# Optimization experiments

Measured on AMD Instinct MI355X. Metric: run time of the kernel, lower is better.

## Reference

```python
import jax, jax.numpy as jnp
import numpy as np

N_SRC = 20000
N_TGT = 20000
N_EDGE = 320000
D = 128            # in_dim == hid_dim
EDGE_IN = 2 * D + 1  # src feat + tgt feat + radial
COORD_MAX = 10.0


def _mlp2(x, w1, b1, w2, b2):
    # Linear -> SiLU -> Linear -> SiLU (edge MLP)
    h = jax.nn.silu(x @ w1 + b1)
    return jax.nn.silu(h @ w2 + b2)


def setup_inputs() -> dict:
    key = jax.random.key(0)
    ks = jax.random.split(key, 32)
    s = 0.05
    inp = {
        "src_node_feat": jax.random.normal(ks[0], (N_SRC, D), jnp.float32),
        "tgt_node_feat": jax.random.normal(ks[1], (N_TGT, D), jnp.float32),
        "src_node_coord": jax.random.normal(ks[2], (N_SRC, 3), jnp.float32),
        "tgt_node_coord": jax.random.normal(ks[3], (N_TGT, 3), jnp.float32),
        "edge_src": jax.random.randint(ks[4], (N_EDGE,), 0, N_SRC, jnp.int32),
        "edge_tgt": jax.random.randint(ks[5], (N_EDGE,), 0, N_TGT, jnp.int32),
        # edge MLP s2t
        "w1_s2t": jax.random.normal(ks[6], (EDGE_IN, D), jnp.float32) * s,
        "b1_s2t": jnp.zeros((D,), jnp.float32),
        "w2_s2t": jax.random.normal(ks[7], (D, D), jnp.float32) * s,
        "b2_s2t": jnp.zeros((D,), jnp.float32),
        # edge MLP t2s
        "w1_t2s": jax.random.normal(ks[8], (EDGE_IN, D), jnp.float32) * s,
        "b1_t2s": jnp.zeros((D,), jnp.float32),
        "w2_t2s": jax.random.normal(ks[9], (D, D), jnp.float32) * s,
        "b2_t2s": jnp.zeros((D,), jnp.float32),
        # gate MLPs (Linear(D,1) + Sigmoid)
        "wg_s2t": jax.random.normal(ks[10], (D, 1), jnp.float32) * s,
        "bg_s2t": jnp.zeros((1,), jnp.float32),
        "wg_t2s": jax.random.normal(ks[11], (D, 1), jnp.float32) * s,
        "bg_t2s": jnp.zeros((1,), jnp.float32),
        # coord MLP: Linear(D,D) + SiLU + Linear(D,1, bias=False, xavier gain 1e-3)
        "wc1": jax.random.normal(ks[12], (D, D), jnp.float32) * s,
        "bc1": jnp.zeros((D,), jnp.float32),
        "wc2": jax.random.normal(ks[13], (D, 1), jnp.float32) * 0.001,
        # node MLP tgt: Linear(2D,D) + SiLU + Linear(D,D)
        "wn1_t": jax.random.normal(ks[14], (2 * D, D), jnp.float32) * s,
        "bn1_t": jnp.zeros((D,), jnp.float32),
        "wn2_t": jax.random.normal(ks[15], (D, D), jnp.float32) * s,
        "bn2_t": jnp.zeros((D,), jnp.float32),
        # node MLP src
        "wn1_s": jax.random.normal(ks[16], (2 * D, D), jnp.float32) * s,
        "bn1_s": jnp.zeros((D,), jnp.float32),
        "wn2_s": jax.random.normal(ks[17], (D, D), jnp.float32) * s,
        "bn2_s": jnp.zeros((D,), jnp.float32),
    }
    return inp


def reference(src_node_feat, tgt_node_feat, src_node_coord, tgt_node_coord,
              edge_src, edge_tgt,
              w1_s2t, b1_s2t, w2_s2t, b2_s2t,
              w1_t2s, b1_t2s, w2_t2s, b2_t2s,
              wg_s2t, bg_s2t, wg_t2s, bg_t2s,
              wc1, bc1, wc2,
              wn1_t, bn1_t, wn2_t, bn2_t,
              wn1_s, bn1_s, wn2_s, bn2_s):
    # ---- coord2radial ----
    coord_diff = tgt_node_coord[edge_tgt] - src_node_coord[edge_src]  # [E,3]
    radial = jnp.sum(coord_diff ** 2, axis=1, keepdims=True)          # [E,1]

    # ---- edge function (gather + concat + two edge MLPs + gates) ----
    edge_in = jnp.concatenate(
        [src_node_feat[edge_src], tgt_node_feat[edge_tgt], radial], axis=1)  # [E, 257]
    e_s2t = _mlp2(edge_in, w1_s2t, b1_s2t, w2_s2t, b2_s2t)  # [E,D]
    e_t2s = _mlp2(edge_in, w1_t2s, b1_t2s, w2_t2s, b2_t2s)  # [E,D]
    e_s2t = e_s2t * jax.nn.sigmoid(e_s2t @ wg_s2t + bg_s2t)
    e_t2s = e_t2s * jax.nn.sigmoid(e_t2s @ wg_t2s + bg_t2s)

    # ---- coord update (coords_agg='mean', output_coord=True) ----
    coord_w = jax.nn.silu(e_s2t @ wc1 + bc1) @ wc2          # [E,1]
    weighted_trans = coord_diff * coord_w                   # [E,3]
    trans_sum = jax.ops.segment_sum(weighted_trans, edge_tgt, num_segments=N_TGT)
    cnt = jax.ops.segment_sum(jnp.ones((weighted_trans.shape[0],), jnp.float32),
                              edge_tgt, num_segments=N_TGT)
    agg_trans = trans_sum / jnp.maximum(cnt, 1.0)[:, None]
    tgt_coord_out = tgt_node_coord + jnp.clip(agg_trans, -COORD_MAX, COORD_MAX)

    # ---- node function (scatter-add aggregation + node MLPs + residual) ----
    agg_s2t = jax.ops.segment_sum(e_s2t, edge_tgt, num_segments=N_TGT)  # [Nt,D]
    agg_t2s = jax.ops.segment_sum(e_t2s, edge_src, num_segments=N_SRC)  # [Ns,D]
    tgt_in = jnp.concatenate([tgt_node_feat, agg_s2t], axis=1)  # [Nt,2D]
    src_in = jnp.concatenate([src_node_feat, agg_t2s], axis=1)  # [Ns,2D]
    tgt_out = jax.nn.silu(tgt_in @ wn1_t + bn1_t) @ wn2_t + bn2_t
    src_out = jax.nn.silu(src_in @ wn1_s + bn1_s) @ wn2_s + bn2_s
    tgt_out = tgt_node_feat + tgt_out  # residual (dims match)
    src_out = src_node_feat + src_out

    return src_out, tgt_out, src_node_coord, tgt_coord_out
```

## Files before the change

### kernel.cpp

```cpp
#include <hip/hip_runtime.h>

#define NN 20000
#define NEDGE 320000
#define COORD_MAX 10.0f

#define LDH 136
#define TILE_N 64
#define LDN  264

typedef __attribute__((ext_vector_type(4))) float f32x4;
typedef __attribute__((ext_vector_type(8))) short short8;
typedef __attribute__((ext_vector_type(8))) __bf16 bf16x8;

static __device__ __forceinline__ f32x4 mfma16(short8 a, short8 b, f32x4 c) {
  return __builtin_amdgcn_mfma_f32_16x16x32_bf16(
      __builtin_bit_cast(bf16x8, a), __builtin_bit_cast(bf16x8, b), c, 0, 0, 0);
}
static __device__ __forceinline__ unsigned short f2bf(float f) {
  unsigned u = __builtin_bit_cast(unsigned, f);
  u += 0x7FFFu + ((u >> 16) & 1u);
  return (unsigned short)(u >> 16);
}
static __device__ __forceinline__ float bf2f(unsigned short u) {
  unsigned x = ((unsigned)u) << 16;
  return __builtin_bit_cast(float, x);
}
static __device__ __forceinline__ unsigned cvtpk(float lo, float hi) {
  unsigned r;
  asm("v_cvt_pk_bf16_f32 %0, %1, %2" : "=v"(r) : "v"(lo), "v"(hi));
  return r;
}
static __device__ __forceinline__ float sigm(float x) {
  return __builtin_amdgcn_rcpf(1.f + __expf(-x));
}
static __device__ __forceinline__ float silu_(float x) { return x * sigm(x); }

struct PackJobs {
  const float* w[11];
  unsigned short* o[11];
  int kreal[11];
  int nk[11];
};

__global__ void egnn_pack_all(PackJobs J) {
  const int job = blockIdx.y;
  const int nk = J.nk[job];
  const int idx = blockIdx.x * 256 + threadIdx.x;
  if (idx >= nk * 512) return;
  const float* w = J.w[job];
  const int kreal = J.kreal[job];
  const int lane = idx & 63;
  const int ct = (idx >> 6) & 7;
  const int kstep = idx >> 9;
  const int col = ct * 16 + (lane & 15);
  const int k0 = kstep * 32 + (lane >> 4) * 8;
  union { short8 s; unsigned short u[8]; } t;
#pragma unroll
  for (int j = 0; j < 8; ++j) {
    int k = k0 + j;
    t.u[j] = (k < kreal) ? f2bf(w[(size_t)k * 128 + col]) : (unsigned short)0;
  }
  reinterpret_cast<short8*>(J.o[job])[idx] = t.s;
}

struct PreJobs {
  const float* x[4];
  const unsigned short* w[4];
  unsigned short* o[4];
};

__global__ __launch_bounds__(256, 2) void egnn_pre(PreJobs J, int N) {
  __shared__ __align__(16) unsigned short sX[64 * LDH];
  const int job = blockIdx.y;
  const float* X = J.x[job];
  const unsigned short* W = J.w[job];
  unsigned short* O = J.o[job];
  const int n0 = blockIdx.x * 64;
  const int tid = threadIdx.x;

  for (int s = tid; s < 64 * 32; s += 256) {
    const int row = s >> 5;
    const int c4 = (s & 31) * 4;
    const int node = n0 + row;
    float4 v = {0.f, 0.f, 0.f, 0.f};
    if (node < N) v = reinterpret_cast<const float4*>(X + (size_t)node * 128)[s & 31];
    *reinterpret_cast<uint2*>(&sX[row * LDH + c4]) =
        uint2{cvtpk(v.x, v.y), cvtpk(v.z, v.w)};
  }
  __syncthreads();

  const int lane = tid & 63, wid = tid >> 6;
  const int r16 = lane & 15, g4 = lane >> 4;
  const int rowBase = wid * 16;

  f32x4 acc[8];
#pragma unroll
  for (int ct = 0; ct < 8; ++ct) acc[ct] = f32x4{0.f, 0.f, 0.f, 0.f};
#pragma unroll
  for (int ks = 0; ks < 4; ++ks) {
    const short8 a = *reinterpret_cast<const short8*>(
        &sX[(rowBase + r16) * LDH + ks * 32 + g4 * 8]);
#pragma unroll
    for (int ct = 0; ct < 8; ++ct) {
      const short8 b = *reinterpret_cast<const short8*>(
          W + ((size_t)(ks * 8 + ct) * 64 + lane) * 8);
      acc[ct] = mfma16(a, b, acc[ct]);
    }
  }
#pragma unroll
  for (int ct = 0; ct < 8; ++ct) {
    const int col = ct * 16 + r16;
#pragma unroll
    for (int r = 0; r < 4; ++r) {
      const int node = n0 + rowBase + g4 * 4 + r;
      if (node < N) O[(size_t)node * 128 + col] = f2bf(acc[ct][r]);
    }
  }
}

__global__ void egnn_hist(const int* __restrict__ eTgt, const int* __restrict__ eSrc,
                          int* __restrict__ cntT, int* __restrict__ cntS) {
  const int e = blockIdx.x * 256 + threadIdx.x;
  if (e < NEDGE) {
    atomicAdd(&cntT[eTgt[e]], 1);
    atomicAdd(&cntS[eSrc[e]], 1);
  }
}

__global__ __launch_bounds__(1024) void egnn_scan(
    const int* __restrict__ c0, int* __restrict__ r0, int* __restrict__ o0,
    const int* __restrict__ c1, int* __restrict__ r1, int* __restrict__ o1, int n) {
  const int* cnt = blockIdx.x ? c1 : c0;
  int* rp = blockIdx.x ? r1 : r0;
  int* oc = blockIdx.x ? o1 : o0;
  __shared__ int sums[1024];
  const int tid = threadIdx.x;
  const int chunk = (n + 1023) / 1024;
  const int i0 = tid * chunk;
  int local = 0;
  for (int k = 0; k < chunk; ++k) {
    const int i = i0 + k;
    if (i < n) local += cnt[i];
  }
  sums[tid] = local;
  __syncthreads();
  for (int s = 1; s < 1024; s <<= 1) {
    int v = (tid >= s) ? sums[tid - s] : 0;
    __syncthreads();
    sums[tid] += v;
    __syncthreads();
  }
  int run = (tid == 0) ? 0 : sums[tid - 1];
  for (int k = 0; k < chunk; ++k) {
    const int i = i0 + k;
    if (i < n) { rp[i] = run; oc[i] = run; run += cnt[i]; }
  }
  if (tid == 1023) rp[n] = sums[1023];
}

__global__ void egnn_scatter(const int* __restrict__ eTgt, const int* __restrict__ eSrc,
                             int* __restrict__ offT, int* __restrict__ offS,
                             int* __restrict__ permT, int* __restrict__ permS) {
  const int e = blockIdx.x * 256 + threadIdx.x;
  if (e < NEDGE) {
    permT[atomicAdd(&offT[eTgt[e]], 1)] = e;
    permS[atomicAdd(&offS[eSrc[e]], 1)] = e;
  }
}

__global__ __launch_bounds__(256, 4) void egnn_edge(
    const unsigned short* __restrict__ S1A, const unsigned short* __restrict__ T1A,
    const unsigned short* __restrict__ S1B, const unsigned short* __restrict__ T1B,
    const float* __restrict__ srcC, const float* __restrict__ tgtC,
    const int* __restrict__ eSrc, const int* __restrict__ eTgt,
    const float* __restrict__ w1A, const float* __restrict__ b1A,
    const float* __restrict__ w1B, const float* __restrict__ b1B,
    const unsigned short* __restrict__ w2pA, const float* __restrict__ b2A,
    const float* __restrict__ wgA, const float* __restrict__ bgA,
    const unsigned short* __restrict__ w2pB, const float* __restrict__ b2B,
    const float* __restrict__ wgB, const float* __restrict__ bgB,
    const unsigned short* __restrict__ wc1p, const float* __restrict__ bc1,
    const float* __restrict__ wc2,
    const int* __restrict__ permT, const int* __restrict__ permS,
    float* __restrict__ aggA, float* __restrict__ aggB,
    float* __restrict__ wtBuf)
{
  __shared__ __align__(16) unsigned short sH[4][32 * LDH];
  __shared__ float sCD[128 * 3];
  __shared__ float sRad[128];
  __shared__ int sS[128];
  __shared__ int sT[128];

  const int dir = blockIdx.y;
  const int tid = threadIdx.x;
  const int j0 = blockIdx.x * 128;
  const int* __restrict__ perm = dir ? permS : permT;

  if (tid < 128) {
    const int e = perm[j0 + tid];
    const int s = eSrc[e], t = eTgt[e];
    sS[tid] = s; sT[tid] = t;
    const float dx = tgtC[t * 3 + 0] - srcC[s * 3 + 0];
    const float dy = tgtC[t * 3 + 1] - srcC[s * 3 + 1];
    const float dz = tgtC[t * 3 + 2] - srcC[s * 3 + 2];
    sCD[tid * 3 + 0] = dx; sCD[tid * 3 + 1] = dy; sCD[tid * 3 + 2] = dz;
    sRad[tid] = dx * dx + dy * dy + dz * dz;
  }
  __syncthreads();

  const int lane = tid & 63, wid = tid >> 6;
  const int r16 = lane & 15, g4 = lane >> 4;
  const int we = wid * 32;
  const int h32 = lane >> 5;
  const int c4 = (lane & 31) * 4;

  const unsigned short* S1 = dir ? S1B : S1A;
  const unsigned short* T1 = dir ? T1B : T1A;
  const float* w1 = dir ? w1B : w1A;
  const float* b1 = dir ? b1B : b1A;
  const float4 wr = *reinterpret_cast<const float4*>(w1 + 256 * 128 + c4);
  const float4 bb = *reinterpret_cast<const float4*>(b1 + c4);

  unsigned short* hT = sH[wid];

#pragma unroll 8
  for (int i = 0; i < 16; ++i) {
    const int row = 2 * i + h32;
    const int e = we + row;
    const int s = sS[e], t = sT[e];
    const float rad = sRad[e];
    const ushort4 a = *reinterpret_cast<const ushort4*>(S1 + (size_t)s * 128 + c4);
    const ushort4 b = *reinterpret_cast<const ushort4*>(T1 + (size_t)t * 128 + c4);
    const float f0 = silu_(bf2f(a.x) + bf2f(b.x) + rad * wr.x + bb.x);
    const float f1 = silu_(bf2f(a.y) + bf2f(b.y) + rad * wr.y + bb.y);
    const float f2 = silu_(bf2f(a.z) + bf2f(b.z) + rad * wr.z + bb.z);
    const float f3 = silu_(bf2f(a.w) + bf2f(b.w) + rad * wr.w + bb.w);
    *reinterpret_cast<uint2*>(&hT[row * LDH + c4]) =
        uint2{cvtpk(f0, f1), cvtpk(f2, f3)};
  }

  const unsigned short* w2p = dir ? w2pB : w2pA;
  f32x4 acc[2][8];
#pragma unroll
  for (int rt = 0; rt < 2; ++rt)
#pragma unroll
    for (int ct = 0; ct < 8; ++ct) acc[rt][ct] = f32x4{0.f, 0.f, 0.f, 0.f};
#pragma unroll
  for (int ks = 0; ks < 4; ++ks) {
    short8 a[2];
#pragma unroll
    for (int rt = 0; rt < 2; ++rt)
      a[rt] = *reinterpret_cast<const short8*>(
          &hT[(rt * 16 + r16) * LDH + ks * 32 + g4 * 8]);
#pragma unroll
    for (int ct = 0; ct < 8; ++ct) {
      const short8 b = *reinterpret_cast<const short8*>(
          w2p + ((size_t)(ks * 8 + ct) * 64 + lane) * 8);
#pragma unroll
      for (int rt = 0; rt < 2; ++rt) acc[rt][ct] = mfma16(a[rt], b, acc[rt][ct]);
    }
  }

  const float* b2 = dir ? b2B : b2A;
  const float* wg = dir ? wgB : wgA;
  const float bg = dir ? bgB[0] : bgA[0];
  float part[2][4];
#pragma unroll
  for (int rt = 0; rt < 2; ++rt)
#pragma unroll
    for (int r = 0; r < 4; ++r) part[rt][r] = 0.f;
#pragma unroll
  for (int ct = 0; ct < 8; ++ct) {
    const float b2v = b2[ct * 16 + r16];
    const float wgv = wg[ct * 16 + r16];
#pragma unroll
    for (int rt = 0; rt < 2; ++rt)
#pragma unroll
      for (int r = 0; r < 4; ++r) {
        const float e = silu_(acc[rt][ct][r] + b2v);
        acc[rt][ct][r] = e;
        part[rt][r] += e * wgv;
      }
  }
#pragma unroll
  for (int m = 1; m < 16; m <<= 1)
#pragma unroll
    for (int rt = 0; rt < 2; ++rt)
#pragma unroll
      for (int r = 0; r < 4; ++r) part[rt][r] += __shfl_xor(part[rt][r], m, 64);
#pragma unroll
  for (int rt = 0; rt < 2; ++rt)
#pragma unroll
    for (int r = 0; r < 4; ++r) {
      const float gate = sigm(part[rt][r] + bg);
#pragma unroll
      for (int ct = 0; ct < 8; ++ct) acc[rt][ct][r] *= gate;
    }

#pragma unroll
  for (int rt = 0; rt < 2; ++rt)
#pragma unroll
    for (int ct = 0; ct < 8; ++ct)
#pragma unroll
      for (int r = 0; r < 4; ++r)
        hT[(rt * 16 + g4 * 4 + r) * LDH + ct * 16 + r16] = f2bf(acc[rt][ct][r]);

  if (dir == 0) {
    f32x4 ac[2][8];
#pragma unroll
    for (int rt = 0; rt < 2; ++rt)
#pragma unroll
      for (int ct = 0; ct < 8; ++ct) ac[rt][ct] = f32x4{0.f, 0.f, 0.f, 0.f};
#pragma unroll
    for (int ks = 0; ks < 4; ++ks) {
      short8 a[2];
#pragma unroll
      for (int rt = 0; rt < 2; ++rt)
        a[rt] = *reinterpret_cast<const short8*>(
            &hT[(rt * 16 + r16) * LDH + ks * 32 + g4 * 8]);
#pragma unroll
      for (int ct = 0; ct < 8; ++ct) {
        const short8 b = *reinterpret_cast<const short8*>(
            wc1p + ((size_t)(ks * 8 + ct) * 64 + lane) * 8);
#pragma unroll
        for (int rt = 0; rt < 2; ++rt) ac[rt][ct] = mfma16(a[rt], b, ac[rt][ct]);
      }
    }
    float pc[2][4];
#pragma unroll
    for (int rt = 0; rt < 2; ++rt)
#pragma unroll
      for (int r = 0; r < 4; ++r) pc[rt][r] = 0.f;
#pragma unroll
    for (int ct = 0; ct < 8; ++ct) {
      const float bcv = bc1[ct * 16 + r16];
      const float w2v = wc2[ct * 16 + r16];
#pragma unroll
      for (int rt = 0; rt < 2; ++rt)
#pragma unroll
        for (int r = 0; r < 4; ++r)
          pc[rt][r] += silu_(ac[rt][ct][r] + bcv) * w2v;
    }
#pragma unroll
    for (int m = 1; m < 16; m <<= 1)
#pragma unroll
      for (int rt = 0; rt < 2; ++rt)
#pragma unroll
        for (int r = 0; r < 4; ++r) pc[rt][r] += __shfl_xor(pc[rt][r], m, 64);

#pragma unroll
    for (int rt = 0; rt < 2; ++rt)
#pragma unroll
      for (int r = 0; r < 4; ++r) {
        if (r16 == 0) {
          const int el = we + rt * 16 + g4 * 4 + r;
          const float p = pc[rt][r];
          const float4 w = {sCD[el * 3 + 0] * p, sCD[el * 3 + 1] * p,
                            sCD[el * 3 + 2] * p, 0.f};
          *reinterpret_cast<float4*>(wtBuf + (size_t)(j0 + el) * 4) = w;
        }
      }
  }

  {
    const int* __restrict__ nids = dir ? sS : sT;
    float* __restrict__ agg = dir ? aggB : aggA;
    const int c2 = lane * 2;
    float s0 = 0.f, s1 = 0.f;
    int curNode = nids[we];
    int segStart = 0;
#pragma unroll 4
    for (int row = 0; row < 32; ++row) {
      const ushort2 v = *reinterpret_cast<const ushort2*>(&hT[row * LDH + c2]);
      s0 += bf2f(v.x); s1 += bf2f(v.y);
      const int nxt = (row < 31) ? nids[we + row + 1] : -1;
      if (nxt != curNode) {
        float* dst = agg + (size_t)curNode * 128 + c2;
        if (segStart > 0 && row < 31) {
          dst[0] = s0; dst[1] = s1;
        } else {
          atomicAdd(dst, s0);
          atomicAdd(dst + 1, s1);
        }
        s0 = 0.f; s1 = 0.f;
        curNode = nxt; segStart = row + 1;
      }
    }
  }
}

__global__ void egnn_coord(const float* __restrict__ srcC, const float* __restrict__ tgtC,
                           const float* __restrict__ wt, const int* __restrict__ rp,
                           float* __restrict__ outSC, float* __restrict__ outTC) {
  const int n = blockIdx.x * 256 + threadIdx.x;
  if (n >= NN) return;
  outSC[n * 3 + 0] = srcC[n * 3 + 0];
  outSC[n * 3 + 1] = srcC[n * 3 + 1];
  outSC[n * 3 + 2] = srcC[n * 3 + 2];
  const int j0 = rp[n], j1 = rp[n + 1];
  float ax = 0.f, ay = 0.f, az = 0.f;
  for (int j = j0; j < j1; ++j) {
    const float4 v = *reinterpret_cast<const float4*>(wt + (size_t)j * 4);
    ax += v.x; ay += v.y; az += v.z;
  }
  const float c = fmaxf((float)(j1 - j0), 1.f);
  ax = fminf(fmaxf(ax / c, -COORD_MAX), COORD_MAX);
  ay = fminf(fmaxf(ay / c, -COORD_MAX), COORD_MAX);
  az = fminf(fmaxf(az / c, -COORD_MAX), COORD_MAX);
  outTC[n * 3 + 0] = tgtC[n * 3 + 0] + ax;
  outTC[n * 3 + 1] = tgtC[n * 3 + 1] + ay;
  outTC[n * 3 + 2] = tgtC[n * 3 + 2] + az;
}

struct NodeJobs {
  const float* feat[2];
  const float* agg[2];
  const unsigned short* w1p[2];
  const float* b1[2];
  const unsigned short* w2p[2];
  const float* b2[2];
  float* outp[2];
};

__global__ __launch_bounds__(256, 2) void egnn_node(NodeJobs J, int N) {
  __shared__ __align__(16) unsigned short sIn[TILE_N * LDN];
  __shared__ __align__(16) unsigned short sH2[TILE_N * LDH];
  const int job = blockIdx.y;
  const float* __restrict__ feat = J.feat[job];
  const float* __restrict__ agg = J.agg[job];
  const unsigned short* __restrict__ w1p = J.w1p[job];
  const float* __restrict__ b1 = J.b1[job];
  const unsigned short* __restrict__ w2p = J.w2p[job];
  const float* __restrict__ b2 = J.b2[job];
  float* __restrict__ outp = J.outp[job];

  const int tid = threadIdx.x;
  const int n0 = blockIdx.x * TILE_N;

  for (int s = tid; s < 64 * 64; s += 256) {
    const int row = s >> 6;
    const int half = (s >> 5) & 1;
    const int c4 = (s & 31) * 4;
    const int node = n0 + row;
    float4 v = {0.f, 0.f, 0.f, 0.f};
    if (node < N)
      v = reinterpret_cast<const float4*>((half ? agg : feat) + (size_t)node * 128)[s & 31];
    *reinterpret_cast<uint2*>(&sIn[row * LDN + half * 128 + c4]) =
        uint2{cvtpk(v.x, v.y), cvtpk(v.z, v.w)};
  }
  __syncthreads();

  const int lane = tid & 63;
  const int wid = tid >> 6;
  const int rowBase = wid * 16;
  const int r16 = lane & 15;
  const int g4 = lane >> 4;

  f32x4 acc[8];
#pragma unroll
  for (int ct = 0; ct < 8; ++ct) acc[ct] = f32x4{0.f, 0.f, 0.f, 0.f};
#pragma unroll
  for (int ks = 0; ks < 8; ++ks) {
    const short8 a = *reinterpret_cast<const short8*>(
        &sIn[(rowBase + r16) * LDN + ks * 32 + g4 * 8]);
#pragma unroll
    for (int ct = 0; ct < 8; ++ct) {
      const short8 b = *reinterpret_cast<const short8*>(
          w1p + ((size_t)(ks * 8 + ct) * 64 + lane) * 8);
      acc[ct] = mfma16(a, b, acc[ct]);
    }
  }
#pragma unroll
  for (int ct = 0; ct < 8; ++ct) {
    const int col = ct * 16 + r16;
    const float bias = b1[col];
#pragma unroll
    for (int r = 0; r < 4; ++r) {
      const float h = silu_(acc[ct][r] + bias);
      sH2[(rowBase + g4 * 4 + r) * LDH + col] = f2bf(h);
    }
  }

  f32x4 acc2[8];
#pragma unroll
  for (int ct = 0; ct < 8; ++ct) acc2[ct] = f32x4{0.f, 0.f, 0.f, 0.f};
#pragma unroll
  for (int ks = 0; ks < 4; ++ks) {
    const short8 a = *reinterpret_cast<const short8*>(
        &sH2[(rowBase + r16) * LDH + ks * 32 + g4 * 8]);
#pragma unroll
    for (int ct = 0; ct < 8; ++ct) {
      const short8 b = *reinterpret_cast<const short8*>(
          w2p + ((size_t)(ks * 8 + ct) * 64 + lane) * 8);
      acc2[ct] = mfma16(a, b, acc2[ct]);
    }
  }

#pragma unroll
  for (int ct = 0; ct < 8; ++ct) {
    const int col = ct * 16 + r16;
    const float bias = b2[col];
#pragma unroll
    for (int r = 0; r < 4; ++r) {
      const int node = n0 + rowBase + g4 * 4 + r;
      if (node < N)
        outp[(size_t)node * 128 + col] = feat[(size_t)node * 128 + col] + acc2[ct][r] + bias;
    }
  }
}

extern "C" void kernel_launch(void* const* d_in, const int* in_sizes, int n_in,
                              void* d_out, int out_size, void* d_ws, size_t ws_size,
                              hipStream_t stream) {
  const float* srcF = (const float*)d_in[0];
  const float* tgtF = (const float*)d_in[1];
  const float* srcC = (const float*)d_in[2];
  const float* tgtC = (const float*)d_in[3];
  const int* eSrc = (const int*)d_in[4];
  const int* eTgt = (const int*)d_in[5];
  const float* w1_s2t = (const float*)d_in[6];
  const float* b1_s2t = (const float*)d_in[7];
  const float* w2_s2t = (const float*)d_in[8];
  const float* b2_s2t = (const float*)d_in[9];
  const float* w1_t2s = (const float*)d_in[10];
  const float* b1_t2s = (const float*)d_in[11];
  const float* w2_t2s = (const float*)d_in[12];
  const float* b2_t2s = (const float*)d_in[13];
  const float* wg_s2t = (const float*)d_in[14];
  const float* bg_s2t = (const float*)d_in[15];
  const float* wg_t2s = (const float*)d_in[16];
  const float* bg_t2s = (const float*)d_in[17];
  const float* wc1 = (const float*)d_in[18];
  const float* bc1 = (const float*)d_in[19];
  const float* wc2 = (const float*)d_in[20];
  const float* wn1_t = (const float*)d_in[21];
  const float* bn1_t = (const float*)d_in[22];
  const float* wn2_t = (const float*)d_in[23];
  const float* bn2_t = (const float*)d_in[24];
  const float* wn1_s = (const float*)d_in[25];
  const float* bn1_s = (const float*)d_in[26];
  const float* wn2_s = (const float*)d_in[27];
  const float* bn2_s = (const float*)d_in[28];

  char* ws = (char*)d_ws;
  size_t off = 0;
  auto take = [&](size_t bytes) -> char* {
    char* p = ws + off;
    off = (off + bytes + 255) & ~(size_t)255;
    return p;
  };
  float* aggA = (float*)take((size_t)NN * 128 * 4);
  float* aggB = (float*)take((size_t)NN * 128 * 4);
  float* wtBuf = (float*)take((size_t)NEDGE * 4 * 4);
  unsigned short* S1A = (unsigned short*)take((size_t)NN * 128 * 2);
  unsigned short* T1A = (unsigned short*)take((size_t)NN * 128 * 2);
  unsigned short* S1B = (unsigned short*)take((size_t)NN * 128 * 2);
  unsigned short* T1B = (unsigned short*)take((size_t)NN * 128 * 2);
  unsigned short* w1tA = (unsigned short*)take(4 * 4096 * 2);
  unsigned short* w1mA = (unsigned short*)take(4 * 4096 * 2);
  unsigned short* w1tB = (unsigned short*)take(4 * 4096 * 2);
  unsigned short* w1mB = (unsigned short*)take(4 * 4096 * 2);
  unsigned short* w2pA = (unsigned short*)take(4 * 4096 * 2);
  unsigned short* w2pB = (unsigned short*)take(4 * 4096 * 2);
  unsigned short* wc1p = (unsigned short*)take(4 * 4096 * 2);
  unsigned short* wn1pt = (unsigned short*)take(8 * 4096 * 2);
  unsigned short* wn2pt = (unsigned short*)take(4 * 4096 * 2);
  unsigned short* wn1ps = (unsigned short*)take(8 * 4096 * 2);
  unsigned short* wn2ps = (unsigned short*)take(4 * 4096 * 2);
  int* cntT = (int*)take((size_t)NN * 4);
  int* cntS = (int*)take((size_t)NN * 4);
  const char* cntZeroStart = (const char*)cntT;
  const size_t cntZeroBytes = (size_t)((char*)cntS + NN * 4 - (char*)cntT);
  int* rowptrT = (int*)take((size_t)(NN + 1) * 4);
  int* rowptrS = (int*)take((size_t)(NN + 1) * 4);
  int* offT = (int*)take((size_t)NN * 4);
  int* offS = (int*)take((size_t)NN * 4);
  int* permT = (int*)take((size_t)NEDGE * 4);
  int* permS = (int*)take((size_t)NEDGE * 4);

  hipMemsetAsync(aggA, 0, (size_t)NN * 128 * 4 * 2, stream);
  hipMemsetAsync((void*)cntZeroStart, 0, cntZeroBytes, stream);

  PackJobs PJ;
  PJ.w[0] = w1_s2t;             PJ.o[0] = w1tA;  PJ.kreal[0] = 128; PJ.nk[0] = 4;
  PJ.w[1] = w1_s2t + 128 * 128; PJ.o[1] = w1mA;  PJ.kreal[1] = 128; PJ.nk[1] = 4;
  PJ.w[2] = w1_t2s;             PJ.o[2] = w1tB;  PJ.kreal[2] = 128; PJ.nk[2] = 4;
  PJ.w[3] = w1_t2s + 128 * 128; PJ.o[3] = w1mB;  PJ.kreal[3] = 128; PJ.nk[3] = 4;
  PJ.w[4] = w2_s2t;             PJ.o[4] = w2pA;  PJ.kreal[4] = 128; PJ.nk[4] = 4;
  PJ.w[5] = w2_t2s;             PJ.o[5] = w2pB;  PJ.kreal[5] = 128; PJ.nk[5] = 4;
  PJ.w[6] = wc1;                PJ.o[6] = wc1p;  PJ.kreal[6] = 128; PJ.nk[6] = 4;
  PJ.w[7] = wn1_t;              PJ.o[7] = wn1pt; PJ.kreal[7] = 256; PJ.nk[7] = 8;
  PJ.w[8] = wn2_t;              PJ.o[8] = wn2pt; PJ.kreal[8] = 128; PJ.nk[8] = 4;
  PJ.w[9] = wn1_s;              PJ.o[9] = wn1ps; PJ.kreal[9] = 256; PJ.nk[9] = 8;
  PJ.w[10] = wn2_s;             PJ.o[10] = wn2ps; PJ.kreal[10] = 128; PJ.nk[10] = 4;
  egnn_pack_all<<<dim3(16, 11), 256, 0, stream>>>(PJ);

  PreJobs PR;
  PR.x[0] = srcF; PR.w[0] = w1tA; PR.o[0] = S1A;
  PR.x[1] = tgtF; PR.w[1] = w1mA; PR.o[1] = T1A;
  PR.x[2] = srcF; PR.w[2] = w1tB; PR.o[2] = S1B;
  PR.x[3] = tgtF; PR.w[3] = w1mB; PR.o[3] = T1B;
  egnn_pre<<<dim3(313, 4), 256, 0, stream>>>(PR, NN);

  egnn_hist<<<NEDGE / 256, 256, 0, stream>>>(eTgt, eSrc, cntT, cntS);
  egnn_scan<<<2, 1024, 0, stream>>>(cntT, rowptrT, offT, cntS, rowptrS, offS, NN);
  egnn_scatter<<<NEDGE / 256, 256, 0, stream>>>(eTgt, eSrc, offT, offS, permT, permS);

  float* outSrc = (float*)d_out;
  float* outTgt = outSrc + (size_t)NN * 128;
  float* outSC  = outTgt + (size_t)NN * 128;
  float* outTC  = outSC + (size_t)NN * 3;

  egnn_edge<<<dim3(NEDGE / 128, 2), 256, 0, stream>>>(
      S1A, T1A, S1B, T1B, srcC, tgtC, eSrc, eTgt,
      w1_s2t, b1_s2t, w1_t2s, b1_t2s,
      w2pA, b2_s2t, wg_s2t, bg_s2t,
      w2pB, b2_t2s, wg_t2s, bg_t2s,
      wc1p, bc1, wc2, permT, permS, aggA, aggB, wtBuf);

  egnn_coord<<<(NN + 255) / 256, 256, 0, stream>>>(
      srcC, tgtC, wtBuf, rowptrT, outSC, outTC);

  NodeJobs NJ;
  NJ.feat[0] = tgtF; NJ.agg[0] = aggA;
  NJ.w1p[0] = wn1pt; NJ.b1[0] = bn1_t; NJ.w2p[0] = wn2pt; NJ.b2[0] = bn2_t;
  NJ.outp[0] = outTgt;
  NJ.feat[1] = srcF; NJ.agg[1] = aggB;
  NJ.w1p[1] = wn1ps; NJ.b1[1] = bn1_s; NJ.w2p[1] = wn2ps; NJ.b2[1] = bn2_s;
  NJ.outp[1] = outSrc;

  const int nodeBlocks = (NN + TILE_N - 1) / TILE_N;
  egnn_node<<<dim3(nodeBlocks, 2), 256, 0, stream>>>(NJ, NN);
}
```

Baseline: 320.9 us.

## Fuse prep kernels, fold bias into pre-GEMM, halve edge tile registers

Merges weight packing, the degree histogram and the agg zeroing into one launch, and drops the memset. The pre-GEMM now computes both directions per block, so the source-feature tile is staged once, and the b1 bias is folded into the target projection. The edge kernel works on 16-row halves with a smaller LDS tile and launch bounds raised to 6 blocks per CU, trading more loop iterations for occupancy. The coordinate kernel is folded into the node kernel as an extra grid row, cutting a launch.

```diff
diff --git a/kernel.cpp b/kernel.cpp
--- a/kernel.cpp
+++ b/kernel.cpp
@@ -42,39 +42,56 @@
   int nk[11];
 };
 
-__global__ void egnn_pack_all(PackJobs J) {
+__global__ void egnn_prep(PackJobs J,
+                          const int* __restrict__ eTgt, const int* __restrict__ eSrc,
+                          int* __restrict__ cntT, int* __restrict__ cntS,
+                          float* __restrict__ aggZero ) {
   const int job = blockIdx.y;
-  const int nk = J.nk[job];
   const int idx = blockIdx.x * 256 + threadIdx.x;
-  if (idx >= nk * 512) return;
-  const float* w = J.w[job];
-  const int kreal = J.kreal[job];
-  const int lane = idx & 63;
-  const int ct = (idx >> 6) & 7;
-  const int kstep = idx >> 9;
-  const int col = ct * 16 + (lane & 15);
-  const int k0 = kstep * 32 + (lane >> 4) * 8;
-  union { short8 s; unsigned short u[8]; } t;
-#pragma unroll
-  for (int j = 0; j < 8; ++j) {
-    int k = k0 + j;
-    t.u[j] = (k < kreal) ? f2bf(w[(size_t)k * 128 + col]) : (unsigned short)0;
-  }
-  reinterpret_cast<short8*>(J.o[job])[idx] = t.s;
+  if (job < 11) {
+    const int nk = J.nk[job];
+    if (idx >= nk * 512) return;
+    const float* w = J.w[job];
+    const int kreal = J.kreal[job];
+    const int lane = idx & 63;
+    const int ct = (idx >> 6) & 7;
+    const int kstep = idx >> 9;
+    const int col = ct * 16 + (lane & 15);
+    const int k0 = kstep * 32 + (lane >> 4) * 8;
+    union { short8 s; unsigned short u[8]; } t;
+#pragma unroll
+    for (int j = 0; j < 8; ++j) {
+      int k = k0 + j;
+      t.u[j] = (k < kreal) ? f2bf(w[(size_t)k * 128 + col]) : (unsigned short)0;
+    }
+    reinterpret_cast<short8*>(J.o[job])[idx] = t.s;
+  } else if (job == 11) {
+    if (idx < NEDGE) {
+      atomicAdd(&cntT[eTgt[idx]], 1);
+      atomicAdd(&cntS[eSrc[idx]], 1);
+    }
+  } else {
+    float4* p = reinterpret_cast<float4*>(aggZero);
+    const int total = 2 * NN * 128 / 4;
+    for (int k = idx; k < total; k += 1250 * 256)
+      p[k] = float4{0.f, 0.f, 0.f, 0.f};
+  }
 }
 
 struct PreJobs {
-  const float* x[4];
-  const unsigned short* w[4];
-  unsigned short* o[4];
+  const float* x[2];
+  const unsigned short* wA[2];
+  const unsigned short* wB[2];
+  const float* biasA[2];
+  const float* biasB[2];
+  unsigned short* oA[2];
+  unsigned short* oB[2];
 };
 
 __global__ __launch_bounds__(256, 2) void egnn_pre(PreJobs J, int N) {
   __shared__ __align__(16) unsigned short sX[64 * LDH];
   const int job = blockIdx.y;
-  const float* X = J.x[job];
-  const unsigned short* W = J.w[job];
-  unsigned short* O = J.o[job];
+  const float* __restrict__ X = J.x[job];
   const int n0 = blockIdx.x * 64;
   const int tid = threadIdx.x;
 
@@ -93,37 +110,35 @@
   const int r16 = lane & 15, g4 = lane >> 4;
   const int rowBase = wid * 16;
 
-  f32x4 acc[8];
-#pragma unroll
-  for (int ct = 0; ct < 8; ++ct) acc[ct] = f32x4{0.f, 0.f, 0.f, 0.f};
-#pragma unroll
-  for (int ks = 0; ks < 4; ++ks) {
-    const short8 a = *reinterpret_cast<const short8*>(
-        &sX[(rowBase + r16) * LDH + ks * 32 + g4 * 8]);
+#pragma unroll 1
+  for (int half = 0; half < 2; ++half) {
+    const unsigned short* __restrict__ W = half ? J.wB[job] : J.wA[job];
+    const float* __restrict__ bias = half ? J.biasB[job] : J.biasA[job];
+    unsigned short* __restrict__ O = half ? J.oB[job] : J.oA[job];
+    f32x4 acc[8];
+#pragma unroll
+    for (int ct = 0; ct < 8; ++ct) acc[ct] = f32x4{0.f, 0.f, 0.f, 0.f};
+#pragma unroll
+    for (int ks = 0; ks < 4; ++ks) {
+      const short8 a = *reinterpret_cast<const short8*>(
+          &sX[(rowBase + r16) * LDH + ks * 32 + g4 * 8]);
+#pragma unroll
+      for (int ct = 0; ct < 8; ++ct) {
+        const short8 b = *reinterpret_cast<const short8*>(
+            W + ((size_t)(ks * 8 + ct) * 64 + lane) * 8);
+        acc[ct] = mfma16(a, b, acc[ct]);
+      }
+    }
 #pragma unroll
     for (int ct = 0; ct < 8; ++ct) {
-      const short8 b = *reinterpret_cast<const short8*>(
-          W + ((size_t)(ks * 8 + ct) * 64 + lane) * 8);
-      acc[ct] = mfma16(a, b, acc[ct]);
-    }
-  }
-#pragma unroll
-  for (int ct = 0; ct < 8; ++ct) {
-    const int col = ct * 16 + r16;
-#pragma unroll
-    for (int r = 0; r < 4; ++r) {
-      const int node = n0 + rowBase + g4 * 4 + r;
-      if (node < N) O[(size_t)node * 128 + col] = f2bf(acc[ct][r]);
-    }
-  }
-}
-
-__global__ void egnn_hist(const int* __restrict__ eTgt, const int* __restrict__ eSrc,
-                          int* __restrict__ cntT, int* __restrict__ cntS) {
-  const int e = blockIdx.x * 256 + threadIdx.x;
-  if (e < NEDGE) {
-    atomicAdd(&cntT[eTgt[e]], 1);
-    atomicAdd(&cntS[eSrc[e]], 1);
+      const int col = ct * 16 + r16;
+      const float bv = bias ? bias[col] : 0.f;
+#pragma unroll
+      for (int r = 0; r < 4; ++r) {
+        const int node = n0 + rowBase + g4 * 4 + r;
+        if (node < N) O[(size_t)node * 128 + col] = f2bf(acc[ct][r] + bv);
+      }
+    }
   }
 }
 
@@ -168,13 +183,12 @@
   }
 }
 
-__global__ __launch_bounds__(256, 4) void egnn_edge(
+__global__ __launch_bounds__(256, 6) void egnn_edge(
     const unsigned short* __restrict__ S1A, const unsigned short* __restrict__ T1A,
     const unsigned short* __restrict__ S1B, const unsigned short* __restrict__ T1B,
     const float* __restrict__ srcC, const float* __restrict__ tgtC,
     const int* __restrict__ eSrc, const int* __restrict__ eTgt,
-    const float* __restrict__ w1A, const float* __restrict__ b1A,
-    const float* __restrict__ w1B, const float* __restrict__ b1B,
+    const float* __restrict__ w1A, const float* __restrict__ w1B,
     const unsigned short* __restrict__ w2pA, const float* __restrict__ b2A,
     const float* __restrict__ wgA, const float* __restrict__ bgA,
     const unsigned short* __restrict__ w2pB, const float* __restrict__ b2B,
@@ -185,7 +199,7 @@
     float* __restrict__ aggA, float* __restrict__ aggB,
     float* __restrict__ wtBuf)
 {
-  __shared__ __align__(16) unsigned short sH[4][32 * LDH];
+  __shared__ __align__(16) unsigned short sH[4][16 * LDH];
   __shared__ float sCD[128 * 3];
   __shared__ float sRad[128];
   __shared__ int sS[128];
@@ -213,165 +227,134 @@
   const int we = wid * 32;
   const int h32 = lane >> 5;
   const int c4 = (lane & 31) * 4;
-
-  const unsigned short* S1 = dir ? S1B : S1A;
-  const unsigned short* T1 = dir ? T1B : T1A;
+  const int c2 = lane * 2;
+
+  const unsigned short* __restrict__ S1 = dir ? S1B : S1A;
+  const unsigned short* __restrict__ T1 = dir ? T1B : T1A;
   const float* w1 = dir ? w1B : w1A;
-  const float* b1 = dir ? b1B : b1A;
   const float4 wr = *reinterpret_cast<const float4*>(w1 + 256 * 128 + c4);
-  const float4 bb = *reinterpret_cast<const float4*>(b1 + c4);
-
-  unsigned short* hT = sH[wid];
-
-#pragma unroll 8
-  for (int i = 0; i < 16; ++i) {
-    const int row = 2 * i + h32;
-    const int e = we + row;
-    const int s = sS[e], t = sT[e];
-    const float rad = sRad[e];
-    const ushort4 a = *reinterpret_cast<const ushort4*>(S1 + (size_t)s * 128 + c4);
-    const ushort4 b = *reinterpret_cast<const ushort4*>(T1 + (size_t)t * 128 + c4);
-    const float f0 = silu_(bf2f(a.x) + bf2f(b.x) + rad * wr.x + bb.x);
-    const float f1 = silu_(bf2f(a.y) + bf2f(b.y) + rad * wr.y + bb.y);
-    const float f2 = silu_(bf2f(a.z) + bf2f(b.z) + rad * wr.z + bb.z);
-    const float f3 = silu_(bf2f(a.w) + bf2f(b.w) + rad * wr.w + bb.w);
-    *reinterpret_cast<uint2*>(&hT[row * LDH + c4]) =
-        uint2{cvtpk(f0, f1), cvtpk(f2, f3)};
-  }
-
-  const unsigned short* w2p = dir ? w2pB : w2pA;
-  f32x4 acc[2][8];
-#pragma unroll
-  for (int rt = 0; rt < 2; ++rt)
-#pragma unroll
-    for (int ct = 0; ct < 8; ++ct) acc[rt][ct] = f32x4{0.f, 0.f, 0.f, 0.f};
-#pragma unroll
-  for (int ks = 0; ks < 4; ++ks) {
-    short8 a[2];
-#pragma unroll
-    for (int rt = 0; rt < 2; ++rt)
-      a[rt] = *reinterpret_cast<const short8*>(
-          &hT[(rt * 16 + r16) * LDH + ks * 32 + g4 * 8]);
-#pragma unroll
-    for (int ct = 0; ct < 8; ++ct) {
-      const short8 b = *reinterpret_cast<const short8*>(
-          w2p + ((size_t)(ks * 8 + ct) * 64 + lane) * 8);
-#pragma unroll
-      for (int rt = 0; rt < 2; ++rt) acc[rt][ct] = mfma16(a[rt], b, acc[rt][ct]);
-    }
-  }
-
   const float* b2 = dir ? b2B : b2A;
   const float* wg = dir ? wgB : wgA;
   const float bg = dir ? bgB[0] : bgA[0];
-  float part[2][4];
-#pragma unroll
-  for (int rt = 0; rt < 2; ++rt)
-#pragma unroll
-    for (int r = 0; r < 4; ++r) part[rt][r] = 0.f;
-#pragma unroll
-  for (int ct = 0; ct < 8; ++ct) {
-    const float b2v = b2[ct * 16 + r16];
-    const float wgv = wg[ct * 16 + r16];
-#pragma unroll
-    for (int rt = 0; rt < 2; ++rt)
-#pragma unroll
-      for (int r = 0; r < 4; ++r) {
-        const float e = silu_(acc[rt][ct][r] + b2v);
-        acc[rt][ct][r] = e;
-        part[rt][r] += e * wgv;
-      }
-  }
-#pragma unroll
-  for (int m = 1; m < 16; m <<= 1)
-#pragma unroll
-    for (int rt = 0; rt < 2; ++rt)
-#pragma unroll
-      for (int r = 0; r < 4; ++r) part[rt][r] += __shfl_xor(part[rt][r], m, 64);
-#pragma unroll
-  for (int rt = 0; rt < 2; ++rt)
-#pragma unroll
-    for (int r = 0; r < 4; ++r) {
-      const float gate = sigm(part[rt][r] + bg);
-#pragma unroll
-      for (int ct = 0; ct < 8; ++ct) acc[rt][ct][r] *= gate;
-    }
-
-#pragma unroll
-  for (int rt = 0; rt < 2; ++rt)
-#pragma unroll
-    for (int ct = 0; ct < 8; ++ct)
-#pragma unroll
-      for (int r = 0; r < 4; ++r)
-        hT[(rt * 16 + g4 * 4 + r) * LDH + ct * 16 + r16] = f2bf(acc[rt][ct][r]);
-
-  if (dir == 0) {
-    f32x4 ac[2][8];
-#pragma unroll
-    for (int rt = 0; rt < 2; ++rt)
-#pragma unroll
-      for (int ct = 0; ct < 8; ++ct) ac[rt][ct] = f32x4{0.f, 0.f, 0.f, 0.f};
+  const int* __restrict__ nids = dir ? sS : sT;
+  float* __restrict__ agg = dir ? aggB : aggA;
+
+  unsigned short* hT = sH[wid];
+
+  float s0 = 0.f, s1 = 0.f;
+  int curNode = nids[we];
+  int segStart = 0;
+
+#pragma unroll 1
+  for (int half = 0; half < 2; ++half) {
+    const int rbase = half * 16;
+
+#pragma unroll
+    for (int i = 0; i < 8; ++i) {
+      const int lrow = 2 * i + h32;
+      const int e = we + rbase + lrow;
+      const int s = sS[e], t = sT[e];
+      const float rad = sRad[e];
+      const ushort4 a = *reinterpret_cast<const ushort4*>(S1 + (size_t)s * 128 + c4);
+      const ushort4 b = *reinterpret_cast<const ushort4*>(T1 + (size_t)t * 128 + c4);
+      const float f0 = silu_(bf2f(a.x) + bf2f(b.x) + rad * wr.x);
+      const float f1 = silu_(bf2f(a.y) + bf2f(b.y) + rad * wr.y);
+      const float f2 = silu_(bf2f(a.z) + bf2f(b.z) + rad * wr.z);
+      const float f3 = silu_(bf2f(a.w) + bf2f(b.w) + rad * wr.w);
+      *reinterpret_cast<uint2*>(&hT[lrow * LDH + c4]) =
+          uint2{cvtpk(f0, f1), cvtpk(f2, f3)};
+    }
+
+    const unsigned short* w2p = dir ? w2pB : w2pA;
+    f32x4 acc[8];
+#pragma unroll
+    for (int ct = 0; ct < 8; ++ct) acc[ct] = f32x4{0.f, 0.f, 0.f, 0.f};
 #pragma unroll
     for (int ks = 0; ks < 4; ++ks) {
-      short8 a[2];
-#pragma unroll
-      for (int rt = 0; rt < 2; ++rt)
-        a[rt] = *reinterpret_cast<const short8*>(
-            &hT[(rt * 16 + r16) * LDH + ks * 32 + g4 * 8]);
+      const short8 a = *reinterpret_cast<const short8*>(
+          &hT[r16 * LDH + ks * 32 + g4 * 8]);
 #pragma unroll
       for (int ct = 0; ct < 8; ++ct) {
         const short8 b = *reinterpret_cast<const short8*>(
-            wc1p + ((size_t)(ks * 8 + ct) * 64 + lane) * 8);
-#pragma unroll
-        for (int rt = 0; rt < 2; ++rt) ac[rt][ct] = mfma16(a[rt], b, ac[rt][ct]);
-      }
-    }
-    float pc[2][4];
-#pragma unroll
-    for (int rt = 0; rt < 2; ++rt)
-#pragma unroll
-      for (int r = 0; r < 4; ++r) pc[rt][r] = 0.f;
+            w2p + ((size_t)(ks * 8 + ct) * 64 + lane) * 8);
+        acc[ct] = mfma16(a, b, acc[ct]);
+      }
+    }
+
+    float part[4] = {0.f, 0.f, 0.f, 0.f};
 #pragma unroll
     for (int ct = 0; ct < 8; ++ct) {
-      const float bcv = bc1[ct * 16 + r16];
-      const float w2v = wc2[ct * 16 + r16];
-#pragma unroll
-      for (int rt = 0; rt < 2; ++rt)
+      const float b2v = b2[ct * 16 + r16];
+      const float wgv = wg[ct * 16 + r16];
+#pragma unroll
+      for (int r = 0; r < 4; ++r) {
+        const float e = silu_(acc[ct][r] + b2v);
+        acc[ct][r] = e;
+        part[r] += e * wgv;
+      }
+    }
+#pragma unroll
+    for (int m = 1; m < 16; m <<= 1)
+#pragma unroll
+      for (int r = 0; r < 4; ++r) part[r] += __shfl_xor(part[r], m, 64);
+#pragma unroll
+    for (int r = 0; r < 4; ++r) {
+      const float gate = sigm(part[r] + bg);
+#pragma unroll
+      for (int ct = 0; ct < 8; ++ct) acc[ct][r] *= gate;
+    }
+
+#pragma unroll
+    for (int ct = 0; ct < 8; ++ct)
+#pragma unroll
+      for (int r = 0; r < 4; ++r)
+        hT[(g4 * 4 + r) * LDH + ct * 16 + r16] = f2bf(acc[ct][r]);
+
+    if (dir == 0) {
+      f32x4 ac[8];
+#pragma unroll
+      for (int ct = 0; ct < 8; ++ct) ac[ct] = f32x4{0.f, 0.f, 0.f, 0.f};
+#pragma unroll
+      for (int ks = 0; ks < 4; ++ks) {
+        const short8 a = *reinterpret_cast<const short8*>(
+            &hT[r16 * LDH + ks * 32 + g4 * 8]);
+#pragma unroll
+        for (int ct = 0; ct < 8; ++ct) {
+          const short8 b = *reinterpret_cast<const short8*>(
+              wc1p + ((size_t)(ks * 8 + ct) * 64 + lane) * 8);
+          ac[ct] = mfma16(a, b, ac[ct]);
+        }
+      }
+      float pc[4] = {0.f, 0.f, 0.f, 0.f};
+#pragma unroll
+      for (int ct = 0; ct < 8; ++ct) {
+        const float bcv = bc1[ct * 16 + r16];
+        const float w2v = wc2[ct * 16 + r16];
 #pragma unroll
         for (int r = 0; r < 4; ++r)
-          pc[rt][r] += silu_(ac[rt][ct][r] + bcv) * w2v;
-    }
-#pragma unroll
-    for (int m = 1; m < 16; m <<= 1)
-#pragma unroll
-      for (int rt = 0; rt < 2; ++rt)
-#pragma unroll
-        for (int r = 0; r < 4; ++r) pc[rt][r] += __shfl_xor(pc[rt][r], m, 64);
-
-#pragma unroll
-    for (int rt = 0; rt < 2; ++rt)
+          pc[r] += silu_(ac[ct][r] + bcv) * w2v;
+      }
+#pragma unroll
+      for (int m = 1; m < 16; m <<= 1)
+#pragma unroll
+        for (int r = 0; r < 4; ++r) pc[r] += __shfl_xor(pc[r], m, 64);
+
 #pragma unroll
       for (int r = 0; r < 4; ++r) {
         if (r16 == 0) {
-          const int el = we + rt * 16 + g4 * 4 + r;
-          const float p = pc[rt][r];
+          const int el = we + rbase + g4 * 4 + r;
+          const float p = pc[r];
           const float4 w = {sCD[el * 3 + 0] * p, sCD[el * 3 + 1] * p,
                             sCD[el * 3 + 2] * p, 0.f};
           *reinterpret_cast<float4*>(wtBuf + (size_t)(j0 + el) * 4) = w;
         }
       }
-  }
-
-  {
-    const int* __restrict__ nids = dir ? sS : sT;
-    float* __restrict__ agg = dir ? aggB : aggA;
-    const int c2 = lane * 2;
-    float s0 = 0.f, s1 = 0.f;
-    int curNode = nids[we];
-    int segStart = 0;
+    }
+
 #pragma unroll 4
-    for (int row = 0; row < 32; ++row) {
-      const ushort2 v = *reinterpret_cast<const ushort2*>(&hT[row * LDH + c2]);
+    for (int lrow = 0; lrow < 16; ++lrow) {
+      const int row = rbase + lrow;
+      const ushort2 v = *reinterpret_cast<const ushort2*>(&hT[lrow * LDH + c2]);
       s0 += bf2f(v.x); s1 += bf2f(v.y);
       const int nxt = (row < 31) ? nids[we + row + 1] : -1;
       if (nxt != curNode) {
@@ -389,29 +372,6 @@
   }
 }
 
-__global__ void egnn_coord(const float* __restrict__ srcC, const float* __restrict__ tgtC,
-                           const float* __restrict__ wt, const int* __restrict__ rp,
-                           float* __restrict__ outSC, float* __restrict__ outTC) {
-  const int n = blockIdx.x * 256 + threadIdx.x;
-  if (n >= NN) return;
-  outSC[n * 3 + 0] = srcC[n * 3 + 0];
-  outSC[n * 3 + 1] = srcC[n * 3 + 1];
-  outSC[n * 3 + 2] = srcC[n * 3 + 2];
-  const int j0 = rp[n], j1 = rp[n + 1];
-  float ax = 0.f, ay = 0.f, az = 0.f;
-  for (int j = j0; j < j1; ++j) {
-    const float4 v = *reinterpret_cast<const float4*>(wt + (size_t)j * 4);
-    ax += v.x; ay += v.y; az += v.z;
-  }
-  const float c = fmaxf((float)(j1 - j0), 1.f);
-  ax = fminf(fmaxf(ax / c, -COORD_MAX), COORD_MAX);
-  ay = fminf(fmaxf(ay / c, -COORD_MAX), COORD_MAX);
-  az = fminf(fmaxf(az / c, -COORD_MAX), COORD_MAX);
-  outTC[n * 3 + 0] = tgtC[n * 3 + 0] + ax;
-  outTC[n * 3 + 1] = tgtC[n * 3 + 1] + ay;
-  outTC[n * 3 + 2] = tgtC[n * 3 + 2] + az;
-}
-
 struct NodeJobs {
   const float* feat[2];
   const float* agg[2];
@@ -422,10 +382,39 @@
   float* outp[2];
 };
 
-__global__ __launch_bounds__(256, 2) void egnn_node(NodeJobs J, int N) {
+__global__ __launch_bounds__(256, 2) void egnn_node(
+    NodeJobs J, int N,
+    const float* __restrict__ srcC, const float* __restrict__ tgtC,
+    const float* __restrict__ wt, const int* __restrict__ rp,
+    float* __restrict__ outSC, float* __restrict__ outTC) {
   __shared__ __align__(16) unsigned short sIn[TILE_N * LDN];
   __shared__ __align__(16) unsigned short sH2[TILE_N * LDH];
   const int job = blockIdx.y;
+  const int tid = threadIdx.x;
+
+  if (job == 2) {
+    const int n = blockIdx.x * 256 + tid;
+    if (n < NN) {
+      outSC[n * 3 + 0] = srcC[n * 3 + 0];
+      outSC[n * 3 + 1] = srcC[n * 3 + 1];
+      outSC[n * 3 + 2] = srcC[n * 3 + 2];
+      const int j0 = rp[n], j1 = rp[n + 1];
+      float ax = 0.f, ay = 0.f, az = 0.f;
+      for (int j = j0; j < j1; ++j) {
+        const float4 v = *reinterpret_cast<const float4*>(wt + (size_t)j * 4);
+        ax += v.x; ay += v.y; az += v.z;
+      }
+      const float c = fmaxf((float)(j1 - j0), 1.f);
+      ax = fminf(fmaxf(ax / c, -COORD_MAX), COORD_MAX);
+      ay = fminf(fmaxf(ay / c, -COORD_MAX), COORD_MAX);
+      az = fminf(fmaxf(az / c, -COORD_MAX), COORD_MAX);
+      outTC[n * 3 + 0] = tgtC[n * 3 + 0] + ax;
+      outTC[n * 3 + 1] = tgtC[n * 3 + 1] + ay;
+      outTC[n * 3 + 2] = tgtC[n * 3 + 2] + az;
+    }
+    return;
+  }
+
   const float* __restrict__ feat = J.feat[job];
   const float* __restrict__ agg = J.agg[job];
   const unsigned short* __restrict__ w1p = J.w1p[job];
@@ -434,7 +423,6 @@
   const float* __restrict__ b2 = J.b2[job];
   float* __restrict__ outp = J.outp[job];
 
-  const int tid = threadIdx.x;
   const int n0 = blockIdx.x * TILE_N;
 
   for (int s = tid; s < 64 * 64; s += 256) {
@@ -578,7 +566,6 @@
   int* permT = (int*)take((size_t)NEDGE * 4);
   int* permS = (int*)take((size_t)NEDGE * 4);
 
-  hipMemsetAsync(aggA, 0, (size_t)NN * 128 * 4 * 2, stream);
   hipMemsetAsync((void*)cntZeroStart, 0, cntZeroBytes, stream);
 
   PackJobs PJ;
@@ -593,16 +580,17 @@
   PJ.w[8] = wn2_t;              PJ.o[8] = wn2pt; PJ.kreal[8] = 128; PJ.nk[8] = 4;
   PJ.w[9] = wn1_s;              PJ.o[9] = wn1ps; PJ.kreal[9] = 256; PJ.nk[9] = 8;
   PJ.w[10] = wn2_s;             PJ.o[10] = wn2ps; PJ.kreal[10] = 128; PJ.nk[10] = 4;
-  egnn_pack_all<<<dim3(16, 11), 256, 0, stream>>>(PJ);
+  egnn_prep<<<dim3(1250, 13), 256, 0, stream>>>(PJ, eTgt, eSrc, cntT, cntS, aggA);
 
   PreJobs PR;
-  PR.x[0] = srcF; PR.w[0] = w1tA; PR.o[0] = S1A;
-  PR.x[1] = tgtF; PR.w[1] = w1mA; PR.o[1] = T1A;
-  PR.x[2] = srcF; PR.w[2] = w1tB; PR.o[2] = S1B;
-  PR.x[3] = tgtF; PR.w[3] = w1mB; PR.o[3] = T1B;
-  egnn_pre<<<dim3(313, 4), 256, 0, stream>>>(PR, NN);
-
-  egnn_hist<<<NEDGE / 256, 256, 0, stream>>>(eTgt, eSrc, cntT, cntS);
+  PR.x[0] = srcF; PR.wA[0] = w1tA; PR.wB[0] = w1tB;
+  PR.biasA[0] = nullptr; PR.biasB[0] = nullptr;
+  PR.oA[0] = S1A; PR.oB[0] = S1B;
+  PR.x[1] = tgtF; PR.wA[1] = w1mA; PR.wB[1] = w1mB;
+  PR.biasA[1] = b1_s2t; PR.biasB[1] = b1_t2s;
+  PR.oA[1] = T1A; PR.oB[1] = T1B;
+  egnn_pre<<<dim3(313, 2), 256, 0, stream>>>(PR, NN);
+
   egnn_scan<<<2, 1024, 0, stream>>>(cntT, rowptrT, offT, cntS, rowptrS, offS, NN);
   egnn_scatter<<<NEDGE / 256, 256, 0, stream>>>(eTgt, eSrc, offT, offS, permT, permS);
 
@@ -613,13 +601,10 @@
 
   egnn_edge<<<dim3(NEDGE / 128, 2), 256, 0, stream>>>(
       S1A, T1A, S1B, T1B, srcC, tgtC, eSrc, eTgt,
-      w1_s2t, b1_s2t, w1_t2s, b1_t2s,
+      w1_s2t, w1_t2s,
       w2pA, b2_s2t, wg_s2t, bg_s2t,
       w2pB, b2_t2s, wg_t2s, bg_t2s,
       wc1p, bc1, wc2, permT, permS, aggA, aggB, wtBuf);
-
-  egnn_coord<<<(NN + 255) / 256, 256, 0, stream>>>(
-      srcC, tgtC, wtBuf, rowptrT, outSC, outTC);
 
   NodeJobs NJ;
   NJ.feat[0] = tgtF; NJ.agg[0] = aggA;
@@ -630,5 +615,6 @@
   NJ.outp[1] = outSrc;
 
   const int nodeBlocks = (NN + TILE_N - 1) / TILE_N;
-  egnn_node<<<dim3(nodeBlocks, 2), 256, 0, stream>>>(NJ, NN);
-}
+  egnn_node<<<dim3(nodeBlocks, 3), 256, 0, stream>>>(
+      NJ, NN, srcC, tgtC, wtBuf, rowptrT, outSC, outTC);
+}
```

Measured after the change: 552.3 us. +72.1%, slower.
